# Kernel tuning notes

Measured on AMD Instinct MI355X. Metric: run time of the kernel, lower is better.

The kernel has to match this reference:

```python
import jax, jax.numpy as jnp
import numpy as np

N = 10000


def gcn_conv(x, W, b, src, dst, n):
    """GCNConv: linear transform then symmetric-normalized aggregation with self-loops."""
    h = x @ W  # [n, out]
    loops = jnp.arange(n, dtype=src.dtype)
    s = jnp.concatenate([src, loops])
    d = jnp.concatenate([dst, loops])
    deg = jnp.zeros((n,), h.dtype).at[d].add(1.0)
    dinv = jax.lax.rsqrt(jnp.maximum(deg, 1.0))
    norm = dinv[s] * dinv[d]  # [E+n]
    out = jax.ops.segment_sum(h[s] * norm[:, None], d, num_segments=n)
    return out + b


def aggr(x1, x2, aw):
    """TwoOrderAggrConv: learned per-channel softmax combine of the two orders."""
    w = jax.nn.softmax(aw, axis=1)  # [C, 2]
    return x1 * w[:, 0] + x2 * w[:, 1]


def setup_inputs() -> dict:
    key = jax.random.key(0)
    ks = jax.random.split(key, 16)

    def glorot(k, shape):
        fan_in, fan_out = shape
        lim = np.sqrt(6.0 / (fan_in + fan_out)).astype(np.float32)
        return jax.random.uniform(k, shape, jnp.float32, -lim, lim)

    inp = {
        'node_feature': jax.random.normal(ks[0], (N, 512), jnp.float32),
        'edge_index1': jax.random.randint(ks[1], (2, 80000), 0, N, jnp.int32),
        'edge_index2': jax.random.randint(ks[2], (2, 160000), 0, N, jnp.int32),
        'W11': glorot(ks[3], (512, 1024)), 'b11': jnp.zeros((1024,), jnp.float32),
        'W12': glorot(ks[4], (512, 1024)), 'b12': jnp.zeros((1024,), jnp.float32),
        'W21': glorot(ks[5], (1024, 512)), 'b21': jnp.zeros((512,), jnp.float32),
        'W22': glorot(ks[6], (1024, 512)), 'b22': jnp.zeros((512,), jnp.float32),
        'W31': glorot(ks[7], (512, 128)), 'b31': jnp.zeros((128,), jnp.float32),
        'W32': glorot(ks[8], (512, 128)), 'b32': jnp.zeros((128,), jnp.float32),
        'aw1': jax.random.normal(ks[9], (1024, 2), jnp.float32) * 0.1,
        'aw2': jax.random.normal(ks[10], (512, 2), jnp.float32) * 0.1,
        'aw3': jax.random.normal(ks[11], (128, 2), jnp.float32) * 0.1,
    }
    return inp


def reference(node_feature, edge_index1, edge_index2,
              W11, b11, W12, b12, W21, b21, W22, b22, W31, b31, W32, b32,
              aw1, aw2, aw3):
    n = node_feature.shape[0]
    s1, d1 = edge_index1[0], edge_index1[1]
    s2, d2 = edge_index2[0], edge_index2[1]
    # dropout in eval mode -> identity
    h1 = jax.nn.elu(gcn_conv(node_feature, W11, b11, s1, d1, n))
    h2 = jax.nn.elu(gcn_conv(node_feature, W12, b12, s2, d2, n))
    h = aggr(h1, h2, aw1)
    h1 = jax.nn.elu(gcn_conv(h, W21, b21, s1, d1, n))
    h2 = jax.nn.elu(gcn_conv(h, W22, b22, s2, d2, n))
    h = aggr(h1, h2, aw2)
    h1 = jax.nn.elu(gcn_conv(h, W31, b31, s1, d1, n))
    h2 = jax.nn.elu(gcn_conv(h, W32, b32, s2, d2, n))
    return aggr(h1, h2, aw3)
```

## Files before the change

### kernel.cpp

```cpp
#include <hip/hip_runtime.h>
#include <hip/hip_bf16.h>
#include <math.h>

using bf16 = __hip_bfloat16;
typedef __attribute__((ext_vector_type(8))) short short8;
typedef __attribute__((ext_vector_type(4))) float floatx4;

__device__ inline void gl_lds16(const void* g, void* l) {
  __builtin_amdgcn_global_load_lds(
      (const __attribute__((address_space(1))) unsigned int*)g,
      (__attribute__((address_space(3))) unsigned int*)l,
      16, 0, 0);
}
__device__ inline float eluf(float x) { return x > 0.f ? x : __expf(x) - 1.f; }
__device__ inline float bf2f(unsigned short h) {
  return __uint_as_float(((unsigned)h) << 16);
}
__device__ inline void bf16x8_fma(short8 r, float w, float* acc) {
#pragma unroll
  for (int k = 0; k < 8; k++) acc[k] += w * bf2f((unsigned short)r[k]);
}

__global__ void probe_dtype(const unsigned short* __restrict__ x, int* __restrict__ flag) {
  __shared__ int s;
  int t = threadIdx.x;
  if (t == 0) s = 0;
  __syncthreads();
  int bad = 0;
  for (int i = t; i < 1024; i += 256) {
    unsigned short h = x[2 * i];
    unsigned e = (h >> 7) & 0xFF;
    if (e >= 0xE5) bad = 1;
  }
  if (bad) atomicOr(&s, 1);
  __syncthreads();
  if (t == 0) flag[0] = s;
}

__global__ void to_bf16_kernel(const void* __restrict__ in, bf16* __restrict__ out,
                               int nelem, const int* __restrict__ flag) {
  int i = blockIdx.x * 256 + threadIdx.x;
  if (i >= nelem) return;
  if (*flag) out[i] = __float2bfloat16(((const float*)in)[i]);
  else       out[i] = ((const bf16*)in)[i];
}

__global__ void small_prep(
    const void* b11, const void* b12, const void* b21, const void* b22,
    const void* b31, const void* b32, const void* aw1, const void* aw2, const void* aw3,
    float* ob11, float* ob12, float* ob21, float* ob22, float* ob31, float* ob32,
    float* ow1, float* ow2, float* ow3, const int* __restrict__ flag) {
  const bool f32 = *flag != 0;
  auto cv = [&](const void* p, int i) -> float {
    return f32 ? ((const float*)p)[i] : __bfloat162float(((const bf16*)p)[i]);
  };
  int t = blockIdx.x * 256 + threadIdx.x;
  if (t < 1024) ob11[t] = cv(b11, t);
  else if (t < 2048) ob12[t - 1024] = cv(b12, t - 1024);
  else if (t < 2560) ob21[t - 2048] = cv(b21, t - 2048);
  else if (t < 3072) ob22[t - 2560] = cv(b22, t - 2560);
  else if (t < 3200) ob31[t - 3072] = cv(b31, t - 3072);
  else if (t < 3328) ob32[t - 3200] = cv(b32, t - 3200);
  else if (t < 4992) {
    int j = t - 3328;
    const void* src; float* dst; int jj;
    if (j < 1024)      { src = aw1; dst = ow1; jj = j; }
    else if (j < 1536) { src = aw2; dst = ow2; jj = j - 1024; }
    else               { src = aw3; dst = ow3; jj = j - 1536; }
    float e0 = cv(src, 2 * jj), e1 = cv(src, 2 * jj + 1);
    float mx = fmaxf(e0, e1);
    float w0 = expf(e0 - mx), w1 = expf(e1 - mx);
    float inv = 1.f / (w0 + w1);
    dst[2 * jj] = w0 * inv;
    dst[2 * jj + 1] = w1 * inv;
  }
}

__global__ void deg_fused(const int* __restrict__ dst1, int E1,
                          const int* __restrict__ dst2, int E2,
                          int* __restrict__ deg1, int* __restrict__ deg2) {
  int e = blockIdx.x * 256 + threadIdx.x;
  if (e < E1) atomicAdd(&deg1[dst1[e]], 1);
  else if (e < E1 + E2) atomicAdd(&deg2[dst2[e - E1]], 1);
}

__global__ void scan2_kernel(const int* __restrict__ deg1, int* __restrict__ off1,
                             float* __restrict__ dinv1,
                             const int* __restrict__ deg2, int* __restrict__ off2,
                             float* __restrict__ dinv2, int n) {
  const int* deg = blockIdx.x ? deg2 : deg1;
  int* off = blockIdx.x ? off2 : off1;
  float* dinv = blockIdx.x ? dinv2 : dinv1;
  __shared__ int s[1024];
  __shared__ int carry_s;
  int t = threadIdx.x;
  if (t == 0) carry_s = 0;
  __syncthreads();
  for (int base = 0; base < n; base += 1024) {
    int i = base + t;
    int orig = (i < n) ? deg[i] : 0;
    s[t] = orig;
    __syncthreads();
    for (int d = 1; d < 1024; d <<= 1) {
      int add = (t >= d) ? s[t - d] : 0;
      __syncthreads();
      s[t] += add;
      __syncthreads();
    }
    int incl = s[t];
    int carry = carry_s;
    if (i < n) {
      off[i]  = carry + incl - orig;
      dinv[i] = rsqrtf((float)(orig + 1));
    }
    __syncthreads();
    if (t == 1023) carry_s = carry + incl;
    __syncthreads();
  }
  if (t == 0) off[n] = carry_s;
}

__global__ void csr_fused(const int* __restrict__ src1, const int* __restrict__ dst1, int E1,
                          const int* __restrict__ src2, const int* __restrict__ dst2, int E2,
                          const int* __restrict__ off1, int* __restrict__ cur1,
                          const float* __restrict__ dinv1,
                          int* __restrict__ cs1, float* __restrict__ cw1,
                          const int* __restrict__ off2, int* __restrict__ cur2,
                          const float* __restrict__ dinv2,
                          int* __restrict__ cs2, float* __restrict__ cw2) {
  int e = blockIdx.x * 256 + threadIdx.x;
  if (e < E1) {
    int d = dst1[e], s = src1[e];
    int slot = off1[d] + atomicAdd(&cur1[d], 1);
    cs1[slot] = s;
    cw1[slot] = dinv1[s];
  } else if (e < E1 + E2) {
    int ee = e - E1;
    int d = dst2[ee], s = src2[ee];
    int slot = off2[d] + atomicAdd(&cur2[d], 1);
    cs2[slot] = s;
    cw2[slot] = dinv2[s];
  }
}

__global__ void transpose_all(const void* W11, const void* W12, const void* W21,
                              const void* W22, const void* W31, const void* W32,
                              bf16* Wt11, bf16* Wt12, bf16* Wt2cat, bf16* Wt3cat,
                              const int* __restrict__ flag) {
  __shared__ bf16 tile[32][33];
  const bool f32 = *flag != 0;
  int b = blockIdx.x;
  const void* in; bf16* out; int K, N, tt;
  if (b < 512)       { in = W11; out = Wt11; K = 512;  N = 1024; tt = b; }
  else if (b < 1024) { in = W12; out = Wt12; K = 512;  N = 1024; tt = b - 512; }
  else if (b < 1536) { in = W21; out = Wt2cat; K = 1024; N = 512; tt = b - 1024; }
  else if (b < 2048) { in = W22; out = Wt2cat + (size_t)512 * 1024; K = 1024; N = 512; tt = b - 1536; }
  else if (b < 2112) { in = W31; out = Wt3cat; K = 512; N = 128; tt = b - 2048; }
  else               { in = W32; out = Wt3cat + (size_t)128 * 512; K = 512; N = 128; tt = b - 2112; }
  int tilesx = N / 32;
  int bx = (tt % tilesx) * 32;
  int by = (tt / tilesx) * 32;
  int tx = threadIdx.x, ty = threadIdx.y;
#pragma unroll
  for (int i = 0; i < 32; i += 8) {
    size_t idx = (size_t)(by + ty + i) * N + (bx + tx);
    tile[ty + i][tx] = f32 ? __float2bfloat16(((const float*)in)[idx])
                           : ((const bf16*)in)[idx];
  }
  __syncthreads();
#pragma unroll
  for (int i = 0; i < 32; i += 8)
    out[(size_t)(bx + ty + i) * K + (by + tx)] = tile[tx][ty + i];
}

__global__ __launch_bounds__(256) void aggx_kernel(
    const bf16* __restrict__ X,
    const int* __restrict__ off1, const int* __restrict__ cs1, const float* __restrict__ cw1,
    const int* __restrict__ off2, const int* __restrict__ cs2, const float* __restrict__ cw2,
    const float* __restrict__ dinv1, const float* __restrict__ dinv2,
    bf16* __restrict__ outA, bf16* __restrict__ outB, int n) {
  int v = blockIdx.x * 4 + (threadIdx.x >> 6);
  if (v >= n) return;
  v = __builtin_amdgcn_readfirstlane(v);
  const int c = (threadIdx.x & 63) * 8;
  const bf16* __restrict__ base = X + c;

  float a[8], b[8];
#pragma unroll
  for (int k = 0; k < 8; k++) { a[k] = 0.f; b[k] = 0.f; }

  int s1 = __builtin_amdgcn_readfirstlane(off1[v]);
  int e1 = __builtin_amdgcn_readfirstlane(off1[v + 1]);
  int i = s1;
  for (; i + 4 <= e1; i += 4) {
    int u0 = cs1[i], u1 = cs1[i + 1], u2 = cs1[i + 2], u3 = cs1[i + 3];
    float w0 = cw1[i], w1 = cw1[i + 1], w2 = cw1[i + 2], w3 = cw1[i + 3];
    short8 r0 = *(const short8*)(base + (size_t)u0 * 512);
    short8 r1 = *(const short8*)(base + (size_t)u1 * 512);
    short8 r2 = *(const short8*)(base + (size_t)u2 * 512);
    short8 r3 = *(const short8*)(base + (size_t)u3 * 512);
    bf16x8_fma(r0, w0, a); bf16x8_fma(r1, w1, a);
    bf16x8_fma(r2, w2, a); bf16x8_fma(r3, w3, a);
  }
  for (; i + 2 <= e1; i += 2) {
    int u0 = cs1[i], u1 = cs1[i + 1];
    float w0 = cw1[i], w1 = cw1[i + 1];
    short8 r0 = *(const short8*)(base + (size_t)u0 * 512);
    short8 r1 = *(const short8*)(base + (size_t)u1 * 512);
    bf16x8_fma(r0, w0, a); bf16x8_fma(r1, w1, a);
  }
  if (i < e1) {
    short8 r0 = *(const short8*)(base + (size_t)cs1[i] * 512);
    bf16x8_fma(r0, cw1[i], a);
  }
  int s2 = __builtin_amdgcn_readfirstlane(off2[v]);
  int e2 = __builtin_amdgcn_readfirstlane(off2[v + 1]);
  i = s2;
  for (; i + 4 <= e2; i += 4) {
    int u0 = cs2[i], u1 = cs2[i + 1], u2 = cs2[i + 2], u3 = cs2[i + 3];
    float w0 = cw2[i], w1 = cw2[i + 1], w2 = cw2[i + 2], w3 = cw2[i + 3];
    short8 r0 = *(const short8*)(base + (size_t)u0 * 512);
    short8 r1 = *(const short8*)(base + (size_t)u1 * 512);
    short8 r2 = *(const short8*)(base + (size_t)u2 * 512);
    short8 r3 = *(const short8*)(base + (size_t)u3 * 512);
    bf16x8_fma(r0, w0, b); bf16x8_fma(r1, w1, b);
    bf16x8_fma(r2, w2, b); bf16x8_fma(r3, w3, b);
  }
  for (; i + 2 <= e2; i += 2) {
    int u0 = cs2[i], u1 = cs2[i + 1];
    float w0 = cw2[i], w1 = cw2[i + 1];
    short8 r0 = *(const short8*)(base + (size_t)u0 * 512);
    short8 r1 = *(const short8*)(base + (size_t)u1 * 512);
    bf16x8_fma(r0, w0, b); bf16x8_fma(r1, w1, b);
  }
  if (i < e2) {
    short8 r0 = *(const short8*)(base + (size_t)cs2[i] * 512);
    bf16x8_fma(r0, cw2[i], b);
  }

  short8 self = *(const short8*)(base + (size_t)v * 512);
  const float dv1 = dinv1[v], dv2 = dinv2[v];
  short8 ra, rb;
#pragma unroll
  for (int k = 0; k < 8; k++) {
    float xs = bf2f((unsigned short)self[k]);
    ra[k] = (short)__bfloat16_as_ushort(__float2bfloat16(dv1 * a[k] + dv1 * dv1 * xs));
    rb[k] = (short)__bfloat16_as_ushort(__float2bfloat16(dv2 * b[k] + dv2 * dv2 * xs));
  }
  *(short8*)(outA + (size_t)v * 512 + c) = ra;
  *(short8*)(outB + (size_t)v * 512 + c) = rb;
}

__device__ inline void gemm_body(const bf16* __restrict__ A, const bf16* __restrict__ Bt,
                                 bf16* __restrict__ C, int M, int K, int N,
                                 int m0, int n0) {
  __shared__ bf16 As[128 * 32];
  __shared__ bf16 Bs[128 * 32];
  const int tid = threadIdx.x;
  const int wave = tid >> 6;
  const int lane = tid & 63;
  const int quad = lane >> 4;
  const int l16 = lane & 15;
  const int wr = (wave >> 1) * 64;
  const int wc = (wave & 1) * 64;
  const int r_sub = lane >> 2;
  const int cb = (lane & 3) * 16;

  floatx4 acc[4][4];
#pragma unroll
  for (int i = 0; i < 4; i++)
#pragma unroll
    for (int j = 0; j < 4; j++) acc[i][j] = (floatx4){0.f, 0.f, 0.f, 0.f};

  for (int k0 = 0; k0 < K; k0 += 32) {
    __syncthreads();
#pragma unroll
    for (int j = 0; j < 2; ++j) {
      int p = wave * 2 + j;
      int ra = p * 16 + r_sub;
      int grow = m0 + ra; if (grow >= M) grow = M - 1;
      gl_lds16((const char*)(A + (size_t)grow * K + k0) + cb, (char*)As + p * 1024);
      int rb = n0 + p * 16 + r_sub;
      gl_lds16((const char*)(Bt + (size_t)rb * K + k0) + cb, (char*)Bs + p * 1024);
    }
    __syncthreads();

    short8 af[4], bfr[4];
#pragma unroll
    for (int i = 0; i < 4; i++)
      af[i] = *(const short8*)(As + (wr + i * 16 + l16) * 32 + quad * 8);
#pragma unroll
    for (int j = 0; j < 4; j++)
      bfr[j] = *(const short8*)(Bs + (wc + j * 16 + l16) * 32 + quad * 8);
#pragma unroll
    for (int i = 0; i < 4; i++)
#pragma unroll
      for (int j = 0; j < 4; j++)
        acc[i][j] = __builtin_amdgcn_mfma_f32_16x16x32_bf16(af[i], bfr[j], acc[i][j], 0, 0, 0);
  }

#pragma unroll
  for (int i = 0; i < 4; i++) {
#pragma unroll
    for (int r = 0; r < 4; r++) {
      int row = m0 + wr + i * 16 + quad * 4 + r;
      if (row < M) {
#pragma unroll
        for (int j = 0; j < 4; j++) {
          int col = n0 + wc + j * 16 + l16;
          C[(size_t)row * N + col] = __float2bfloat16(acc[i][j][r]);
        }
      }
    }
  }
}

__global__ __launch_bounds__(256) void gemm128_sw(
    const bf16* __restrict__ A0, const bf16* __restrict__ Bt0, bf16* __restrict__ C0,
    const bf16* __restrict__ A1, const bf16* __restrict__ Bt1, bf16* __restrict__ C1,
    int M, int K, int N, int mtilesPerHalf, int mtTotal, int ntLog2) {
  int lin = blockIdx.x;
  int g = lin & 7;
  int s = lin >> 3;
  int n_t = s & ((1 << ntLog2) - 1);
  int m_t = g + 8 * (s >> ntLog2);
  if (m_t >= mtTotal) return;
  int half = (m_t >= mtilesPerHalf) ? 1 : 0;
  int m_local = m_t - half * mtilesPerHalf;
  const bf16* A = half ? A1 : A0;
  const bf16* Bt = half ? Bt1 : Bt0;
  bf16* C = half ? C1 : C0;
  gemm_body(A, Bt, C, M, K, N, m_local * 128, n_t * 128);
}

__global__ __launch_bounds__(256) void combine1_kernel(
    const bf16* __restrict__ Ha, const bf16* __restrict__ Hb,
    const float* __restrict__ ba, const float* __restrict__ bb,
    const float* __restrict__ w01, bf16* __restrict__ out, int total) {
  int e = (blockIdx.x * 256 + threadIdx.x) * 8;
  if (e >= total) return;
  int c = e & 1023;
  short8 ha = *(const short8*)(Ha + e);
  short8 hb = *(const short8*)(Hb + e);
  short8 r;
#pragma unroll
  for (int k = 0; k < 8; k++) {
    float x = eluf(bf2f((unsigned short)ha[k]) + ba[c + k]);
    float y = eluf(bf2f((unsigned short)hb[k]) + bb[c + k]);
    r[k] = (short)__bfloat16_as_ushort(
        __float2bfloat16(x * w01[2 * (c + k)] + y * w01[2 * (c + k) + 1]));
  }
  *(short8*)(out + e) = r;
}

template <int C, bool WU>
__global__ __launch_bounds__(256) void agg_out_kernel(
    const bf16* __restrict__ Ha, const bf16* __restrict__ Hb, int ldH,
    const int* __restrict__ off1, const int* __restrict__ cs1, const float* __restrict__ cw1,
    const int* __restrict__ off2, const int* __restrict__ cs2, const float* __restrict__ cw2,
    const float* __restrict__ dinv1, const float* __restrict__ dinv2,
    const float* __restrict__ ba, const float* __restrict__ bb,
    const float* __restrict__ w01, void* __restrict__ out, int n,
    const int* __restrict__ outflag) {
  constexpr int TPV = C / 8;
  constexpr int G = 256 / TPV;
  const int t = threadIdx.x;
  int v = blockIdx.x * G + t / TPV;
  if (v >= n) return;
  if (WU) v = __builtin_amdgcn_readfirstlane(v);
  const int c = (t % TPV) * 8;
  const bf16* __restrict__ baseA = Ha + c;
  const bf16* __restrict__ baseB = Hb + c;

  float a[8], b[8];
#pragma unroll
  for (int k = 0; k < 8; k++) { a[k] = 0.f; b[k] = 0.f; }

  int s1 = off1[v], e1 = off1[v + 1];
  if (WU) { s1 = __builtin_amdgcn_readfirstlane(s1); e1 = __builtin_amdgcn_readfirstlane(e1); }
  int i = s1;
  for (; i + 4 <= e1; i += 4) {
    int u0 = cs1[i], u1 = cs1[i + 1], u2 = cs1[i + 2], u3 = cs1[i + 3];
    float w0 = cw1[i], w1 = cw1[i + 1], w2 = cw1[i + 2], w3 = cw1[i + 3];
    short8 r0 = *(const short8*)(baseA + (size_t)u0 * ldH);
    short8 r1 = *(const short8*)(baseA + (size_t)u1 * ldH);
    short8 r2 = *(const short8*)(baseA + (size_t)u2 * ldH);
    short8 r3 = *(const short8*)(baseA + (size_t)u3 * ldH);
    bf16x8_fma(r0, w0, a); bf16x8_fma(r1, w1, a);
    bf16x8_fma(r2, w2, a); bf16x8_fma(r3, w3, a);
  }
  for (; i + 2 <= e1; i += 2) {
    int u0 = cs1[i], u1 = cs1[i + 1];
    float w0 = cw1[i], w1 = cw1[i + 1];
    short8 r0 = *(const short8*)(baseA + (size_t)u0 * ldH);
    short8 r1 = *(const short8*)(baseA + (size_t)u1 * ldH);
    bf16x8_fma(r0, w0, a); bf16x8_fma(r1, w1, a);
  }
  if (i < e1) {
    short8 r0 = *(const short8*)(baseA + (size_t)cs1[i] * ldH);
    bf16x8_fma(r0, cw1[i], a);
  }
  int s2 = off2[v], e2 = off2[v + 1];
  if (WU) { s2 = __builtin_amdgcn_readfirstlane(s2); e2 = __builtin_amdgcn_readfirstlane(e2); }
  i = s2;
  for (; i + 4 <= e2; i += 4) {
    int u0 = cs2[i], u1 = cs2[i + 1], u2 = cs2[i + 2], u3 = cs2[i + 3];
    float w0 = cw2[i], w1 = cw2[i + 1], w2 = cw2[i + 2], w3 = cw2[i + 3];
    short8 r0 = *(const short8*)(baseB + (size_t)u0 * ldH);
    short8 r1 = *(const short8*)(baseB + (size_t)u1 * ldH);
    short8 r2 = *(const short8*)(baseB + (size_t)u2 * ldH);
    short8 r3 = *(const short8*)(baseB + (size_t)u3 * ldH);
    bf16x8_fma(r0, w0, b); bf16x8_fma(r1, w1, b);
    bf16x8_fma(r2, w2, b); bf16x8_fma(r3, w3, b);
  }
  for (; i + 2 <= e2; i += 2) {
    int u0 = cs2[i], u1 = cs2[i + 1];
    float w0 = cw2[i], w1 = cw2[i + 1];
    short8 r0 = *(const short8*)(baseB + (size_t)u0 * ldH);
    short8 r1 = *(const short8*)(baseB + (size_t)u1 * ldH);
    bf16x8_fma(r0, w0, b); bf16x8_fma(r1, w1, b);
  }
  if (i < e2) {
    short8 r0 = *(const short8*)(baseB + (size_t)cs2[i] * ldH);
    bf16x8_fma(r0, cw2[i], b);
  }

  short8 sa = *(const short8*)(baseA + (size_t)v * ldH);
  short8 sb = *(const short8*)(baseB + (size_t)v * ldH);
  const float dv1 = dinv1[v], dv2 = dinv2[v];

  float r[8];
#pragma unroll
  for (int k = 0; k < 8; k++) {
    float x = eluf(dv1 * a[k] + dv1 * dv1 * bf2f((unsigned short)sa[k]) + ba[c + k]);
    float y = eluf(dv2 * b[k] + dv2 * dv2 * bf2f((unsigned short)sb[k]) + bb[c + k]);
    r[k] = x * w01[2 * (c + k)] + y * w01[2 * (c + k) + 1];
  }

  const bool out_f32 = (outflag != nullptr) && (*outflag != 0);
  size_t oi = (size_t)v * C + c;
  if (out_f32) {
    floatx4 lo = {r[0], r[1], r[2], r[3]};
    floatx4 hi = {r[4], r[5], r[6], r[7]};
    *(floatx4*)((float*)out + oi) = lo;
    *(floatx4*)((float*)out + oi + 4) = hi;
  } else {
    short8 rb;
#pragma unroll
    for (int k = 0; k < 8; k++)
      rb[k] = (short)__bfloat16_as_ushort(__float2bfloat16(r[k]));
    *(short8*)((bf16*)out + oi) = rb;
  }
}

extern "C" void kernel_launch(void* const* d_in, const int* in_sizes, int n_in,
                              void* d_out, int out_size, void* d_ws, size_t ws_size,
                              hipStream_t stream) {
  const void* X = d_in[0];
  const int* ei1 = (const int*)d_in[1];
  const int* ei2 = (const int*)d_in[2];
  const int n = in_sizes[0] / 512;
  const int E1 = in_sizes[1] / 2;
  const int E2 = in_sizes[2] / 2;
  const int* src1 = ei1;           const int* dst1 = ei1 + E1;
  const int* src2 = ei2;           const int* dst2 = ei2 + E2;

  auto rnd = [](size_t b) { return (b + 255) & ~(size_t)255; };
  char* p = (char*)d_ws;
  auto alloc = [&](size_t bytes) { char* r = p; p += rnd(bytes); return r; };

  int* flag = (int*)alloc(256);
  int* deg1 = (int*)alloc((size_t)n * 4);
  int* deg2 = (int*)alloc((size_t)n * 4);
  int* cur1 = (int*)alloc((size_t)n * 4);
  int* cur2 = (int*)alloc((size_t)n * 4);
  int* off1 = (int*)alloc((size_t)(n + 1) * 4);
  int* off2 = (int*)alloc((size_t)(n + 1) * 4);
  float* dinv1 = (float*)alloc((size_t)n * 4);
  float* dinv2 = (float*)alloc((size_t)n * 4);
  int* cs1 = (int*)alloc((size_t)E1 * 4);
  float* cw1 = (float*)alloc((size_t)E1 * 4);
  int* cs2 = (int*)alloc((size_t)E2 * 4);
  float* cw2 = (float*)alloc((size_t)E2 * 4);
  bf16* Wt11 = (bf16*)alloc((size_t)512 * 1024 * 2);
  bf16* Wt12 = (bf16*)alloc((size_t)512 * 1024 * 2);
  bf16* Wt2cat = (bf16*)alloc((size_t)1024 * 1024 * 2);
  bf16* Wt3cat = (bf16*)alloc((size_t)256 * 512 * 2);
  float* bf_[6]; int bsz[6] = {1024, 1024, 512, 512, 128, 128};
  for (int i = 0; i < 6; i++) bf_[i] = (float*)alloc((size_t)bsz[i] * 4);
  float* w01_[3]; int asz[3] = {2048, 1024, 256};
  for (int i = 0; i < 3; i++) w01_[i] = (float*)alloc((size_t)asz[i] * 4);
  bf16* Xb = (bf16*)alloc((size_t)n * 512 * 2);
  bf16* aggXa = (bf16*)alloc((size_t)n * 512 * 2);
  bf16* aggXb = (bf16*)alloc((size_t)n * 512 * 2);
  bf16* H1a = (bf16*)alloc((size_t)n * 1024 * 2);
  bf16* H1b = (bf16*)alloc((size_t)n * 1024 * 2);
  bf16* act1 = (bf16*)alloc((size_t)n * 1024 * 2);
  bf16* H2cat = H1a;
  bf16* act2 = aggXa;
  bf16* H3cat = H1b;

  probe_dtype<<<1, 256, 0, stream>>>((const unsigned short*)X, flag);
  hipMemsetAsync(deg1, 0, rnd((size_t)n * 4) * 4, stream);

  to_bf16_kernel<<<(n * 512 + 255) / 256, 256, 0, stream>>>(X, Xb, n * 512, flag);
  small_prep<<<20, 256, 0, stream>>>(d_in[4], d_in[6], d_in[8], d_in[10], d_in[12], d_in[14],
                                     d_in[15], d_in[16], d_in[17],
                                     bf_[0], bf_[1], bf_[2], bf_[3], bf_[4], bf_[5],
                                     w01_[0], w01_[1], w01_[2], flag);

  int Etot = E1 + E2;
  deg_fused<<<(Etot + 255) / 256, 256, 0, stream>>>(dst1, E1, dst2, E2, deg1, deg2);
  scan2_kernel<<<2, 1024, 0, stream>>>(deg1, off1, dinv1, deg2, off2, dinv2, n);
  csr_fused<<<(Etot + 255) / 256, 256, 0, stream>>>(src1, dst1, E1, src2, dst2, E2,
                                                    off1, cur1, dinv1, cs1, cw1,
                                                    off2, cur2, dinv2, cs2, cw2);

  transpose_all<<<2176, dim3(32, 8), 0, stream>>>(d_in[3], d_in[5], d_in[7], d_in[9],
                                                  d_in[11], d_in[13],
                                                  Wt11, Wt12, Wt2cat, Wt3cat, flag);

  const int mtiles = (n + 127) / 128;
  auto swgrid = [](int mtTotal, int ntiles) {
    return 8 * ntiles * ((mtTotal + 7) / 8);
  };
  aggx_kernel<<<(n + 3) / 4, 256, 0, stream>>>(Xb, off1, cs1, cw1, off2, cs2, cw2,
                                               dinv1, dinv2, aggXa, aggXb, n);
  gemm128_sw<<<swgrid(2 * mtiles, 8), 256, 0, stream>>>(
      aggXa, Wt11, H1a, aggXb, Wt12, H1b, n, 512, 1024, mtiles, 2 * mtiles, 3);
  combine1_kernel<<<(n * 1024 / 8 + 255) / 256, 256, 0, stream>>>(
      H1a, H1b, bf_[0], bf_[1], w01_[0], act1, n * 1024);
  gemm128_sw<<<swgrid(mtiles, 8), 256, 0, stream>>>(
      act1, Wt2cat, H2cat, act1, Wt2cat, H2cat, n, 1024, 1024, mtiles, mtiles, 3);
  agg_out_kernel<512, true><<<(n + 3) / 4, 256, 0, stream>>>(
      H2cat, H2cat + 512, 1024, off1, cs1, cw1, off2, cs2, cw2,
      dinv1, dinv2, bf_[2], bf_[3], w01_[1], act2, n, (const int*)nullptr);
  gemm128_sw<<<swgrid(mtiles, 2), 256, 0, stream>>>(
      act2, Wt3cat, H3cat, act2, Wt3cat, H3cat, n, 512, 256, mtiles, mtiles, 1);
  agg_out_kernel<128, false><<<(n + 15) / 16, 256, 0, stream>>>(
      H3cat, H3cat + 128, 256, off1, cs1, cw1, off2, cs2, cw2,
      dinv1, dinv2, bf_[4], bf_[5], w01_[2], d_out, n, flag);
}
```

Baseline: 345.3 us.

## Fuse prep kernels into one launch and swizzle GEMM LDS reads

Merges dtype probe with the degree-buffer zeroing, and folds weight transpose, input bf16 conversion (now vectorized 8-wide), bias/softmax prep and degree counting into one multi-role kernel. The aim is to cut launch count and serialization among the small setup kernels. Separately, the GEMM's LDS fragment reads now use an XOR swizzle on the column chunk to reduce bank conflicts. The swizzle is applied to the reads and to `cb`, so correctness depends on the LDS store path using `cb` consistently. The transpose branch also gains an odd null check on X.

Result: faster. 328.9 us (-4.8%).

```diff
diff --git a/kernel.cpp b/kernel.cpp
--- a/kernel.cpp
+++ b/kernel.cpp
@@ -21,67 +21,118 @@
   for (int k = 0; k < 8; k++) acc[k] += w * bf2f((unsigned short)r[k]);
 }
 
-__global__ void probe_dtype(const unsigned short* __restrict__ x, int* __restrict__ flag) {
-  __shared__ int s;
-  int t = threadIdx.x;
-  if (t == 0) s = 0;
-  __syncthreads();
-  int bad = 0;
-  for (int i = t; i < 1024; i += 256) {
-    unsigned short h = x[2 * i];
-    unsigned e = (h >> 7) & 0xFF;
-    if (e >= 0xE5) bad = 1;
-  }
-  if (bad) atomicOr(&s, 1);
-  __syncthreads();
-  if (t == 0) flag[0] = s;
-}
-
-__global__ void to_bf16_kernel(const void* __restrict__ in, bf16* __restrict__ out,
-                               int nelem, const int* __restrict__ flag) {
-  int i = blockIdx.x * 256 + threadIdx.x;
-  if (i >= nelem) return;
-  if (*flag) out[i] = __float2bfloat16(((const float*)in)[i]);
-  else       out[i] = ((const bf16*)in)[i];
-}
-
-__global__ void small_prep(
+__global__ void probe_zero(const unsigned short* __restrict__ x, int* __restrict__ flag,
+                           int* __restrict__ zbase, int zwords) {
+  if (blockIdx.x == 0) {
+    __shared__ int s;
+    int t = threadIdx.x;
+    if (t == 0) s = 0;
+    __syncthreads();
+    int bad = 0;
+    for (int i = t; i < 1024; i += 256) {
+      unsigned short h = x[2 * i];
+      unsigned e = (h >> 7) & 0xFF;
+      if (e >= 0xE5) bad = 1;
+    }
+    if (bad) atomicOr(&s, 1);
+    __syncthreads();
+    if (t == 0) flag[0] = s;
+  } else {
+    int i = (blockIdx.x - 1) * 1024 + threadIdx.x * 4;
+    if (i < zwords) {
+      zbase[i] = 0; zbase[i + 1] = 0; zbase[i + 2] = 0; zbase[i + 3] = 0;
+    }
+  }
+}
+
+__global__ void prep_all(
+    const void* X, bf16* __restrict__ Xb, int nx,
+    const void* W11, const void* W12, const void* W21, const void* W22,
+    const void* W31, const void* W32,
+    bf16* Wt11, bf16* Wt12, bf16* Wt2cat, bf16* Wt3cat,
     const void* b11, const void* b12, const void* b21, const void* b22,
     const void* b31, const void* b32, const void* aw1, const void* aw2, const void* aw3,
     float* ob11, float* ob12, float* ob21, float* ob22, float* ob31, float* ob32,
-    float* ow1, float* ow2, float* ow3, const int* __restrict__ flag) {
+    float* ow1, float* ow2, float* ow3,
+    const int* __restrict__ dst1, int E1, const int* __restrict__ dst2, int E2,
+    int* __restrict__ deg1, int* __restrict__ deg2,
+    const int* __restrict__ flag) {
   const bool f32 = *flag != 0;
-  auto cv = [&](const void* p, int i) -> float {
-    return f32 ? ((const float*)p)[i] : __bfloat162float(((const bf16*)p)[i]);
-  };
-  int t = blockIdx.x * 256 + threadIdx.x;
-  if (t < 1024) ob11[t] = cv(b11, t);
-  else if (t < 2048) ob12[t - 1024] = cv(b12, t - 1024);
-  else if (t < 2560) ob21[t - 2048] = cv(b21, t - 2048);
-  else if (t < 3072) ob22[t - 2560] = cv(b22, t - 2560);
-  else if (t < 3200) ob31[t - 3072] = cv(b31, t - 3072);
-  else if (t < 3328) ob32[t - 3200] = cv(b32, t - 3200);
-  else if (t < 4992) {
-    int j = t - 3328;
-    const void* src; float* dst; int jj;
-    if (j < 1024)      { src = aw1; dst = ow1; jj = j; }
-    else if (j < 1536) { src = aw2; dst = ow2; jj = j - 1024; }
-    else               { src = aw3; dst = ow3; jj = j - 1536; }
-    float e0 = cv(src, 2 * jj), e1 = cv(src, 2 * jj + 1);
-    float mx = fmaxf(e0, e1);
-    float w0 = expf(e0 - mx), w1 = expf(e1 - mx);
-    float inv = 1.f / (w0 + w1);
-    dst[2 * jj] = w0 * inv;
-    dst[2 * jj + 1] = w1 * inv;
-  }
-}
-
-__global__ void deg_fused(const int* __restrict__ dst1, int E1,
-                          const int* __restrict__ dst2, int E2,
-                          int* __restrict__ deg1, int* __restrict__ deg2) {
-  int e = blockIdx.x * 256 + threadIdx.x;
-  if (e < E1) atomicAdd(&deg1[dst1[e]], 1);
-  else if (e < E1 + E2) atomicAdd(&deg2[dst2[e - E1]], 1);
+  int b = blockIdx.x;
+  const int xbBlocks = nx / 2048;
+  if (b < 2176) {
+    __shared__ bf16 tile[32][33];
+    const void* in; bf16* out; int K, N, tt;
+    if (b < 512)       { in = W11; out = Wt11; K = 512;  N = 1024; tt = b; }
+    else if (b < 1024) { in = W12; out = Wt12; K = 512;  N = 1024; tt = b - 512; }
+    else if (b < 1536) { in = W21; out = Wt2cat; K = 1024; N = 512; tt = b - 1024; }
+    else if (b < 2048) { in = W22; out = Wt2cat + (size_t)512 * 1024; K = 1024; N = 512; tt = b - 1536; }
+    else if (b < 2112) { in = W31; out = Wt3cat; K = 512; N = 128; tt = b - 2048; }
+    else               { in = W32; out = Wt3cat + (size_t)128 * 512; K = 512; N = 128; tt = b - 2112; }
+    int tilesx = N / 32;
+    int bx = (tt % tilesx) * 32;
+    int by = (tt / tilesx) * 32;
+    int tx = threadIdx.x & 31, ty = threadIdx.x >> 5;
+#pragma unroll
+    for (int i = 0; i < 32; i += 8) {
+      size_t idx = (size_t)(by + ty + i) * N + (bx + tx);
+      tile[ty + i][tx] = f32 ? __float2bfloat16(((const float*)X == nullptr ? 0.f : ((const float*)in)[idx]))
+                             : ((const bf16*)in)[idx];
+    }
+    __syncthreads();
+#pragma unroll
+    for (int i = 0; i < 32; i += 8)
+      out[(size_t)(bx + ty + i) * K + (by + tx)] = tile[tx][ty + i];
+    return;
+  }
+  b -= 2176;
+  if (b < xbBlocks) {
+    int e = (b * 256 + threadIdx.x) * 8;
+    if (f32) {
+      const float* src = (const float*)X + e;
+      short8 r;
+#pragma unroll
+      for (int k = 0; k < 8; k++)
+        r[k] = (short)__bfloat16_as_ushort(__float2bfloat16(src[k]));
+      *(short8*)(Xb + e) = r;
+    } else {
+      *(short8*)(Xb + e) = *(const short8*)((const bf16*)X + e);
+    }
+    return;
+  }
+  b -= xbBlocks;
+  if (b < 20) {
+    auto cv = [&](const void* p, int i) -> float {
+      return f32 ? ((const float*)p)[i] : __bfloat162float(((const bf16*)p)[i]);
+    };
+    int t = b * 256 + threadIdx.x;
+    if (t < 1024) ob11[t] = cv(b11, t);
+    else if (t < 2048) ob12[t - 1024] = cv(b12, t - 1024);
+    else if (t < 2560) ob21[t - 2048] = cv(b21, t - 2048);
+    else if (t < 3072) ob22[t - 2560] = cv(b22, t - 2560);
+    else if (t < 3200) ob31[t - 3072] = cv(b31, t - 3072);
+    else if (t < 3328) ob32[t - 3200] = cv(b32, t - 3200);
+    else if (t < 4992) {
+      int j = t - 3328;
+      const void* src; float* dst; int jj;
+      if (j < 1024)      { src = aw1; dst = ow1; jj = j; }
+      else if (j < 1536) { src = aw2; dst = ow2; jj = j - 1024; }
+      else               { src = aw3; dst = ow3; jj = j - 1536; }
+      float e0 = cv(src, 2 * jj), e1 = cv(src, 2 * jj + 1);
+      float mx = fmaxf(e0, e1);
+      float w0 = expf(e0 - mx), w1 = expf(e1 - mx);
+      float inv = 1.f / (w0 + w1);
+      dst[2 * jj] = w0 * inv;
+      dst[2 * jj + 1] = w1 * inv;
+    }
+    return;
+  }
+  b -= 20;
+  {
+    int e = b * 256 + threadIdx.x;
+    if (e < E1) atomicAdd(&deg1[dst1[e]], 1);
+    else if (e < E1 + E2) atomicAdd(&deg2[dst2[e - E1]], 1);
+  }
 }
 
 __global__ void scan2_kernel(const int* __restrict__ deg1, int* __restrict__ off1,
@@ -143,36 +194,6 @@
   }
 }
 
-__global__ void transpose_all(const void* W11, const void* W12, const void* W21,
-                              const void* W22, const void* W31, const void* W32,
-                              bf16* Wt11, bf16* Wt12, bf16* Wt2cat, bf16* Wt3cat,
-                              const int* __restrict__ flag) {
-  __shared__ bf16 tile[32][33];
-  const bool f32 = *flag != 0;
-  int b = blockIdx.x;
-  const void* in; bf16* out; int K, N, tt;
-  if (b < 512)       { in = W11; out = Wt11; K = 512;  N = 1024; tt = b; }
-  else if (b < 1024) { in = W12; out = Wt12; K = 512;  N = 1024; tt = b - 512; }
-  else if (b < 1536) { in = W21; out = Wt2cat; K = 1024; N = 512; tt = b - 1024; }
-  else if (b < 2048) { in = W22; out = Wt2cat + (size_t)512 * 1024; K = 1024; N = 512; tt = b - 1536; }
-  else if (b < 2112) { in = W31; out = Wt3cat; K = 512; N = 128; tt = b - 2048; }
-  else               { in = W32; out = Wt3cat + (size_t)128 * 512; K = 512; N = 128; tt = b - 2112; }
-  int tilesx = N / 32;
-  int bx = (tt % tilesx) * 32;
-  int by = (tt / tilesx) * 32;
-  int tx = threadIdx.x, ty = threadIdx.y;
-#pragma unroll
-  for (int i = 0; i < 32; i += 8) {
-    size_t idx = (size_t)(by + ty + i) * N + (bx + tx);
-    tile[ty + i][tx] = f32 ? __float2bfloat16(((const float*)in)[idx])
-                           : ((const bf16*)in)[idx];
-  }
-  __syncthreads();
-#pragma unroll
-  for (int i = 0; i < 32; i += 8)
-    out[(size_t)(bx + ty + i) * K + (by + tx)] = tile[tx][ty + i];
-}
-
 __global__ __launch_bounds__(256) void aggx_kernel(
     const bf16* __restrict__ X,
     const int* __restrict__ off1, const int* __restrict__ cs1, const float* __restrict__ cw1,
@@ -264,7 +285,8 @@
   const int wr = (wave >> 1) * 64;
   const int wc = (wave & 1) * 64;
   const int r_sub = lane >> 2;
-  const int cb = (lane & 3) * 16;
+  const int cb = (((lane & 3) ^ ((lane >> 3) & 3)) * 16);
+  const int rsw = (l16 >> 1) & 3;
 
   floatx4 acc[4][4];
 #pragma unroll
@@ -288,10 +310,10 @@
     short8 af[4], bfr[4];
 #pragma unroll
     for (int i = 0; i < 4; i++)
-      af[i] = *(const short8*)(As + (wr + i * 16 + l16) * 32 + quad * 8);
+      af[i] = *(const short8*)(As + (wr + i * 16 + l16) * 32 + (quad ^ rsw) * 8);
 #pragma unroll
     for (int j = 0; j < 4; j++)
-      bfr[j] = *(const short8*)(Bs + (wc + j * 16 + l16) * 32 + quad * 8);
+      bfr[j] = *(const short8*)(Bs + (wc + j * 16 + l16) * 32 + (quad ^ rsw) * 8);
 #pragma unroll
     for (int i = 0; i < 4; i++)
 #pragma unroll
@@ -500,25 +522,26 @@
   bf16* act2 = aggXa;
   bf16* H3cat = H1b;
 
-  probe_dtype<<<1, 256, 0, stream>>>((const unsigned short*)X, flag);
-  hipMemsetAsync(deg1, 0, rnd((size_t)n * 4) * 4, stream);
-
-  to_bf16_kernel<<<(n * 512 + 255) / 256, 256, 0, stream>>>(X, Xb, n * 512, flag);
-  small_prep<<<20, 256, 0, stream>>>(d_in[4], d_in[6], d_in[8], d_in[10], d_in[12], d_in[14],
-                                     d_in[15], d_in[16], d_in[17],
-                                     bf_[0], bf_[1], bf_[2], bf_[3], bf_[4], bf_[5],
-                                     w01_[0], w01_[1], w01_[2], flag);
-
-  int Etot = E1 + E2;
-  deg_fused<<<(Etot + 255) / 256, 256, 0, stream>>>(dst1, E1, dst2, E2, deg1, deg2);
+  int zwords = (int)(rnd((size_t)n * 4) * 4 / 4);
+  probe_zero<<<1 + (zwords + 1023) / 1024, 256, 0, stream>>>(
+      (const unsigned short*)X, flag, deg1, zwords);
+
+  int xbBlocks = (n * 512) / 2048;
+  int degBlocks = (E1 + E2 + 255) / 256;
+  prep_all<<<2176 + xbBlocks + 20 + degBlocks, 256, 0, stream>>>(
+      X, Xb, n * 512,
+      d_in[3], d_in[5], d_in[7], d_in[9], d_in[11], d_in[13],
+      Wt11, Wt12, Wt2cat, Wt3cat,
+      d_in[4], d_in[6], d_in[8], d_in[10], d_in[12], d_in[14],
+      d_in[15], d_in[16], d_in[17],
+      bf_[0], bf_[1], bf_[2], bf_[3], bf_[4], bf_[5],
+      w01_[0], w01_[1], w01_[2],
+      dst1, E1, dst2, E2, deg1, deg2, flag);
+
   scan2_kernel<<<2, 1024, 0, stream>>>(deg1, off1, dinv1, deg2, off2, dinv2, n);
-  csr_fused<<<(Etot + 255) / 256, 256, 0, stream>>>(src1, dst1, E1, src2, dst2, E2,
-                                                    off1, cur1, dinv1, cs1, cw1,
-                                                    off2, cur2, dinv2, cs2, cw2);
-
-  transpose_all<<<2176, dim3(32, 8), 0, stream>>>(d_in[3], d_in[5], d_in[7], d_in[9],
-                                                  d_in[11], d_in[13],
-                                                  Wt11, Wt12, Wt2cat, Wt3cat, flag);
+  csr_fused<<<(E1 + E2 + 255) / 256, 256, 0, stream>>>(src1, dst1, E1, src2, dst2, E2,
+                                                       off1, cur1, dinv1, cs1, cw1,
+                                                       off2, cur2, dinv2, cs2, cw2);
 
   const int mtiles = (n + 127) / 128;
   auto swgrid = [](int mtTotal, int ntiles) {
```
